# Performance work log

Hardware: AMD Instinct MI355X
Metric: run time of the kernel (lower is better)

Reference implementation:

```python
import jax, jax.numpy as jnp
import numpy as np

ALPHA = 0.3
B, T = 512, 65536


def setup_inputs() -> dict:
    key = jax.random.key(0)
    # F0 values roughly in a vocal pitch range; uniform fill per spec
    f0_frames = jax.random.uniform(key, (B, T), dtype=jnp.float32)
    return {"f0_frames": f0_frames}


def reference(f0_frames):
    # EMA: y[t] = alpha*x[t] + (1-alpha)*y[t-1], with y_prev initialized to x[:,0]
    # (so y[0] == x[0], matching the torch loop).
    alpha = jnp.float32(ALPHA)
    one_m_alpha = jnp.float32(1.0 - ALPHA)
    x_t = jnp.swapaxes(f0_frames, 0, 1)  # (T, B) for scan over time

    def step(carry, x):
        y = alpha * x + one_m_alpha * carry
        return y, y

    _, ys = jax.lax.scan(step, x_t[0], x_t)  # ys: (T, B)
    return jnp.swapaxes(ys, 0, 1)  # (B, T)
```

## Files before the change

kernel.cpp:

```cpp
#include <hip/hip_runtime.h>


#define AL  0.3f
#define BE  0.7f
#define Q4  0.2401f
#define Q8  0.05764801f
#define Q16 0.0033232931f
#define LOG2_07_X4 -2.0582926913190332f
#define BLOCK 256
#define NI  16
#define WCH 256
#define SEG (NI * WCH)

typedef float floatx4 __attribute__((ext_vector_type(4)));

__device__ __forceinline__ float masked_ks(float lend, int lane) {
  float s = lend;
  float t = __shfl_up(s, 1, 64); if (lane < 1) t = 0.f;
  s = fmaf(Q4, t, s);
  t = __shfl_up(s, 2, 64);      if (lane < 2) t = 0.f;
  s = fmaf(Q8, t, s);
  t = __shfl_up(s, 4, 64);      if (lane < 4) t = 0.f;
  s = fmaf(Q16, t, s);
  return s;
}

__global__ __launch_bounds__(BLOCK, 8) void ema_kernel(
    const float* __restrict__ x, float* __restrict__ y, int T) {
  const int tid  = threadIdx.x;
  const int lane = tid & 63;
  const int gw   = blockIdx.x * (BLOCK / 64) + (tid >> 6);
  const int row  = gw >> 4;
  const int seg  = (gw & 15) * SEG;
  const size_t rowoff = (size_t)row * (size_t)T;
  const float* xrow = x + rowoff;
  float*       yrow = y + rowoff;
  const int lb = lane * 4;

  const float pw = exp2f(LOG2_07_X4 * (float)lane);

  floatx4 a = *(const floatx4*)(xrow + seg + lb);
  float seed;
  if (seg == 0) {
    seed = __shfl(a[0], 0, 64);
  } else {
    const floatx4 h = *(const floatx4*)(xrow + seg - WCH + lb);
    float c = 0.f;
    c = fmaf(AL, h[0], BE * c);
    c = fmaf(AL, h[1], BE * c);
    c = fmaf(AL, h[2], BE * c);
    c = fmaf(AL, h[3], BE * c);
    seed = __shfl(masked_ks(c, lane), 63, 64);
  }

#pragma unroll
  for (int ci = 0; ci < NI; ++ci) {
    floatx4 nx;
    if (ci + 1 < NI)
      nx = *(const floatx4*)(xrow + seg + (ci + 1) * WCH + lb);

    float c = 0.f;
    c = fmaf(AL, a[0], BE * c); a[0] = c;
    c = fmaf(AL, a[1], BE * c); a[1] = c;
    c = fmaf(AL, a[2], BE * c); a[2] = c;
    c = fmaf(AL, a[3], BE * c); a[3] = c;

    const float s = masked_ks(c, lane);
    float sp = __shfl_up(s, 1, 64); if (lane == 0) sp = 0.f;
    const float cin = fmaf(pw, seed, sp);

    a[0] = fmaf(cin, 0.7f,    a[0]);
    a[1] = fmaf(cin, 0.49f,   a[1]);
    a[2] = fmaf(cin, 0.343f,  a[2]);
    a[3] = fmaf(cin, 0.2401f, a[3]);

    __builtin_nontemporal_store(a, (floatx4*)(yrow + seg + ci * WCH + lb));

    seed = __shfl(s, 63, 64);
    a = nx;
  }
}

extern "C" void kernel_launch(void* const* d_in, const int* in_sizes, int n_in,
                              void* d_out, int out_size, void* d_ws, size_t ws_size,
                              hipStream_t stream) {
  const float* x = (const float*)d_in[0];
  float* y = (float*)d_out;

  const int T = 65536;
  const int B = in_sizes[0] / T;
  const int wavesTotal = B * (T / SEG);
  const int grid = wavesTotal / (BLOCK / 64);

  ema_kernel<<<grid, BLOCK, 0, stream>>>(x, y, T);
}
```

Measured before the change: 45.82 us.

## Halve segment length per wave and deepen load prefetch to two chunks

Each wave now processes 8 chunks instead of 16, so there are twice as many waves and more parallelism is exposed. The load pipeline is deepened from one chunk ahead to two chunks ahead to hide more memory latency. The cost is more halo reads (one extra chunk per segment) and higher register pressure from the extra prefetch buffer.

After: 45.29 us. Within noise of the previous version (-1.2%).

```diff
diff --git a/kernel.cpp b/kernel.cpp
--- a/kernel.cpp
+++ b/kernel.cpp
@@ -8,7 +8,7 @@
 #define Q16 0.0033232931f
 #define LOG2_07_X4 -2.0582926913190332f
 #define BLOCK 256
-#define NI  16
+#define NI  8
 #define WCH 256
 #define SEG (NI * WCH)
 
@@ -30,21 +30,25 @@
   const int tid  = threadIdx.x;
   const int lane = tid & 63;
   const int gw   = blockIdx.x * (BLOCK / 64) + (tid >> 6);
-  const int row  = gw >> 4;
-  const int seg  = (gw & 15) * SEG;
+  const int segsPerRow = 65536 / SEG;
+  const int row  = gw >> 5;
+  const int seg  = (gw & (segsPerRow - 1)) * SEG;
   const size_t rowoff = (size_t)row * (size_t)T;
   const float* xrow = x + rowoff;
   float*       yrow = y + rowoff;
   const int lb = lane * 4;
+  const float* ps = xrow + seg;
+
+  floatx4 cur = *(const floatx4*)(ps + lb);
+  floatx4 n1  = *(const floatx4*)(ps + WCH + lb);
 
   const float pw = exp2f(LOG2_07_X4 * (float)lane);
 
-  floatx4 a = *(const floatx4*)(xrow + seg + lb);
   float seed;
   if (seg == 0) {
-    seed = __shfl(a[0], 0, 64);
+    seed = __shfl(cur[0], 0, 64);
   } else {
-    const floatx4 h = *(const floatx4*)(xrow + seg - WCH + lb);
+    const floatx4 h = *(const floatx4*)(ps - WCH + lb);
     float c = 0.f;
     c = fmaf(AL, h[0], BE * c);
     c = fmaf(AL, h[1], BE * c);
@@ -55,29 +59,30 @@
 
 #pragma unroll
   for (int ci = 0; ci < NI; ++ci) {
-    floatx4 nx;
-    if (ci + 1 < NI)
-      nx = *(const floatx4*)(xrow + seg + (ci + 1) * WCH + lb);
+    floatx4 n2;
+    if (ci + 2 < NI)
+      n2 = *(const floatx4*)(ps + (ci + 2) * WCH + lb);
 
     float c = 0.f;
-    c = fmaf(AL, a[0], BE * c); a[0] = c;
-    c = fmaf(AL, a[1], BE * c); a[1] = c;
-    c = fmaf(AL, a[2], BE * c); a[2] = c;
-    c = fmaf(AL, a[3], BE * c); a[3] = c;
+    c = fmaf(AL, cur[0], BE * c); cur[0] = c;
+    c = fmaf(AL, cur[1], BE * c); cur[1] = c;
+    c = fmaf(AL, cur[2], BE * c); cur[2] = c;
+    c = fmaf(AL, cur[3], BE * c); cur[3] = c;
 
     const float s = masked_ks(c, lane);
     float sp = __shfl_up(s, 1, 64); if (lane == 0) sp = 0.f;
     const float cin = fmaf(pw, seed, sp);
 
-    a[0] = fmaf(cin, 0.7f,    a[0]);
-    a[1] = fmaf(cin, 0.49f,   a[1]);
-    a[2] = fmaf(cin, 0.343f,  a[2]);
-    a[3] = fmaf(cin, 0.2401f, a[3]);
+    cur[0] = fmaf(cin, 0.7f,    cur[0]);
+    cur[1] = fmaf(cin, 0.49f,   cur[1]);
+    cur[2] = fmaf(cin, 0.343f,  cur[2]);
+    cur[3] = fmaf(cin, 0.2401f, cur[3]);
 
-    __builtin_nontemporal_store(a, (floatx4*)(yrow + seg + ci * WCH + lb));
+    __builtin_nontemporal_store(cur, (floatx4*)(yrow + seg + ci * WCH + lb));
 
     seed = __shfl(s, 63, 64);
-    a = nx;
+    cur = n1;
+    n1 = n2;
   }
 }
 
```
